# Optimization experiments

Measured on AMD Instinct MI355X. Metric: run time of the kernel, lower is better.

Reference implementation:

```python
import jax, jax.numpy as jnp
import numpy as np

RES = 320
B = 32

def make_trajectory():
    # Faithful to get_init_trajectory_full: grid points (i,j), zeroed inside the
    # skip bands (i in [140,170] OR j in [120,160]), then shifted by -res/2.
    I, J = np.meshgrid(np.arange(RES), np.arange(RES), indexing='ij')
    pts = np.stack([I, J], axis=-1).astype(np.float32)
    skip = ((I >= 140) & (I <= 170)) | ((J >= 120) & (J <= 160))
    pts[skip] = 0.0
    pts = pts.reshape(-1, 2) - 0.5 * RES
    return jnp.asarray(pts)

def setup_inputs():
    key = jax.random.key(0)
    k_space_input = jax.random.normal(key, (B, 1, RES, RES, 2), dtype=jnp.float32)
    trajectory = make_trajectory()
    return {"k_space_input": k_space_input, "trajectory": trajectory}

def _forward(k_space_input, trajectory):
    H = W = RES
    b = k_space_input.shape[0]
    # [B,1,H,W,2] -> permute(0,1,4,2,3).squeeze(1) -> [B,2,H,W]
    ksp = jnp.transpose(k_space_input[:, 0], (0, 3, 1, 2))
    c = ksp[:, 0] + 1j * ksp[:, 1]                       # [B,H,W] complex k-space

    # --- bilinear grid-sample at trajectory points (zero padding, align_corners=False) ---
    g = trajectory * (2.0 / W)                           # normalize [-res/2,res/2] -> [-1,1]
    x = ((g[:, 0] + 1.0) * W - 1.0) * 0.5                # pixel x (width)
    y = ((g[:, 1] + 1.0) * H - 1.0) * 0.5                # pixel y (height)
    x0f = jnp.floor(x); y0f = jnp.floor(y)
    fx = x - x0f; fy = y - y0f
    x0 = x0f.astype(jnp.int32); y0 = y0f.astype(jnp.int32)
    corners = ((x0,     y0,     (1 - fx) * (1 - fy)),
               (x0 + 1, y0,     fx       * (1 - fy)),
               (x0,     y0 + 1, (1 - fx) * fy),
               (x0 + 1, y0 + 1, fx       * fy))

    def gather(ix, iy):
        valid = (ix >= 0) & (ix < W) & (iy >= 0) & (iy < H)
        v = c[:, jnp.clip(iy, 0, H - 1), jnp.clip(ix, 0, W - 1)]   # [B,N]
        return jnp.where(valid[None, :], v, 0.0)

    sub = sum(gather(ix, iy) * w[None, :] for ix, iy, w in corners)  # [B,N] sampled k-space

    # --- NUFFT adjoint: bilinear gridding (adjoint scatter-add) + centered inverse FFT ---
    grid = jnp.zeros((b, H * W), dtype=sub.dtype)
    for ix, iy, w in corners:
        valid = (ix >= 0) & (ix < W) & (iy >= 0) & (iy < H)
        idx = jnp.clip(iy, 0, H - 1) * W + jnp.clip(ix, 0, W - 1)
        grid = grid.at[:, idx].add(sub * jnp.where(valid, w, 0.0)[None, :])
    kgrid = grid.reshape(b, H, W)
    img = jnp.fft.fftshift(
        jnp.fft.ifft2(jnp.fft.ifftshift(kgrid, axes=(-2, -1)), axes=(-2, -1)),
        axes=(-2, -1)) * (H * W)                          # adjoint DFT = N * centered ifft
    out = jnp.stack([img.real, img.imag], axis=1)         # [B,2,H,W]
    return out[:, None]                                   # unsqueeze(1) -> [B,1,2,H,W]

def reference(k_space_input, trajectory):
    return _forward(k_space_input, trajectory)
```

## Files before the change

### kernel.cpp

```cpp
#include <hip/hip_runtime.h>

#define RES 320
#define CELLS (RES * RES)
#define MDIM 640
#define NCOLS 10240
#define UF 192

#define DEGC 1360.625f

typedef __attribute__((ext_vector_type(8))) short short8;
typedef __attribute__((ext_vector_type(4))) float f32x4;

static __device__ __forceinline__ short f2bf(float f) {
    unsigned u = __builtin_bit_cast(unsigned, f);
    unsigned r = (u + 0x7fffu + ((u >> 16) & 1u)) >> 16;
    return (short)r;
}

#define GLD16(g, l) __builtin_amdgcn_global_load_lds(                        \
    (const __attribute__((address_space(1))) void*)(g),                      \
    (__attribute__((address_space(3))) void*)(l), 16, 0, 0)

__global__ __launch_bounds__(256) void gen_fafb(short* __restrict__ FBf,
                                                short* __restrict__ FAf) {
    int idx = blockIdx.x * 256 + threadIdx.x;
    int mat = idx / (2 * UF * RES);
    int r = idx - mat * (2 * UF * RES);
    int row = r / RES, c = r % RES;
    int plane = row >= UF;
    int n = row - UF * plane;
    float vr = 0.f;
    if (n <= 160) {
        int lo = mat ? 120 : 140, hi = mat ? 160 : 170;
#pragma unroll
        for (int dx = -1; dx <= 1; dx++) {
            int xx = c - dx;
            if (xx < 0 || xx > RES - 1) continue;
            int a0 = (xx < lo || xx > hi) ? 1 : 0;
            int a1 = (xx + 1 <= RES - 1 && (xx + 1 < lo || xx + 1 > hi)) ? 1 : 0;
            float w;
            if (dx == -1) w = (xx >= 1) ? (float)a0 : 0.f;
            else if (dx == 0) w = (float)(a0 + ((xx <= RES - 2) ? a1 : 0));
            else w = (xx <= RES - 2) ? (float)a1 : 0.f;
            if (w != 0.f) {
                int rr = (n * xx) % RES;
                float s, cc;
                sincospif((float)rr * (2.0f / RES), &s, &cc);
                float sign = ((n + xx) & 1) ? -1.0f : 1.0f;
                vr += w * sign * (plane ? s : cc);
            }
        }
        if (mat == 0) vr *= 0.0625f;
    }
    (mat ? FAf : FBf)[r] = f2bf(vr);
}

__global__ __launch_bounds__(256) void gemm1(const short* __restrict__ FBf,
                                             const float2* __restrict__ ksp,
                                             short* __restrict__ T) {
    __shared__ __align__(16) union {
        struct { short At[2][128 * 32]; short Bt[2][128 * 40]; } s;
        float Q[2][64 * 64];
    } sm;
    int tid = threadIdx.x;
    int lane = tid & 63, wave = tid >> 6;
    int wr = wave >> 1, wc = wave & 1;
    int d = blockIdx.x;
    int xcd = d & 7, rblk = d >> 3;
    int b = xcd * 4 + rblk / 15;
    int t5 = rblk % 15;
    int v0 = (t5 / 5) * 64;
    int y0b = (t5 % 5) * 64;
    const float2* kb = ksp + (size_t)b * CELLS;
    int q = lane >> 4, tl = lane & 15;
    int row4 = tid >> 2, ko = (tid & 3) * 8;
    int brow = tid >> 2, bxq = (tid & 3) * 8;
    f32x4 acc[4][4];
#pragma unroll
    for (int i = 0; i < 4; i++)
#pragma unroll
        for (int j = 0; j < 4; j++) acc[i][j] = {0.f, 0.f, 0.f, 0.f};

#define S1A(buf, k0)                                                         \
    {                                                                        \
        GLD16(FBf + (size_t)(v0 + row4) * RES + (k0) + ko,                   \
              sm.s.At[buf] + (size_t)(wave * 64) * 8);                       \
        GLD16(FBf + (size_t)(UF + v0 + row4) * RES + (k0) + ko,              \
              sm.s.At[buf] + (size_t)(256 + wave * 64) * 8);                 \
    }

    float2 bv[8];
#define S1BLOAD(k0)                                                          \
    {                                                                        \
        const float2* src = kb + (size_t)(y0b + brow) * RES + (k0) + bxq;    \
        _Pragma("unroll") for (int e = 0; e < 8; e++) bv[e] = src[e];        \
    }
#define S1BWRITE(buf)                                                        \
    {                                                                        \
        short8 r8, i8;                                                       \
        _Pragma("unroll") for (int e = 0; e < 8; e++) {                      \
            r8[e] = f2bf(bv[e].x);                                           \
            i8[e] = f2bf(bv[e].y);                                           \
        }                                                                    \
        *(short8*)&sm.s.Bt[buf][brow * 40 + bxq] = r8;                       \
        *(short8*)&sm.s.Bt[buf][(64 + brow) * 40 + bxq] = i8;                \
    }

    S1A(0, 0);
    S1BLOAD(0);
    S1BWRITE(0);
    __syncthreads();
    int cur = 0;
    for (int kt = 0; kt < 10; kt++) {
        if (kt < 9) {
            S1A(cur ^ 1, (kt + 1) * 32);
            S1BLOAD((kt + 1) * 32);
        }
        short8 a[4], bf[4];
#pragma unroll
        for (int i = 0; i < 4; i++)
            a[i] = *(const short8*)&sm.s.At[cur][(wr * 64 + i * 16 + tl) * 32 + q * 8];
#pragma unroll
        for (int j = 0; j < 4; j++)
            bf[j] = *(const short8*)&sm.s.Bt[cur][(wc * 64 + j * 16 + tl) * 40 + q * 8];
#pragma unroll
        for (int i = 0; i < 4; i++)
#pragma unroll
            for (int j = 0; j < 4; j++)
                acc[i][j] = __builtin_amdgcn_mfma_f32_16x16x32_bf16(a[i], bf[j], acc[i][j], 0, 0, 0);
        if (kt < 9) S1BWRITE(cur ^ 1);
        __syncthreads();
        cur ^= 1;
    }
    if (wave == 1 || wave == 3) {
        float* dst = sm.Q[wave >> 1];
#pragma unroll
        for (int i = 0; i < 4; i++)
#pragma unroll
            for (int j = 0; j < 4; j++)
#pragma unroll
                for (int t = 0; t < 4; t++)
                    dst[(i * 16 + q * 4 + t) * 64 + j * 16 + tl] = acc[i][j][t];
    }
    __syncthreads();
    if (wave == 0) {
#pragma unroll
        for (int i = 0; i < 4; i++)
#pragma unroll
            for (int j = 0; j < 4; j++)
#pragma unroll
                for (int t = 0; t < 4; t++) {
                    int r = i * 16 + q * 4 + t, cl = j * 16 + tl;
                    int n = v0 + r, y = y0b + cl;
                    float q11 = sm.Q[1][r * 64 + cl];
                    if (n <= 160)
                        T[(size_t)(b * RES + n) * MDIM + y] = f2bf(acc[i][j][t] - q11);
                    if (n >= 1 && n <= 159)
                        T[(size_t)(b * RES + RES - n) * MDIM + y] = f2bf(acc[i][j][t] + q11);
                }
    } else if (wave == 2) {
#pragma unroll
        for (int i = 0; i < 4; i++)
#pragma unroll
            for (int j = 0; j < 4; j++)
#pragma unroll
                for (int t = 0; t < 4; t++) {
                    int r = i * 16 + q * 4 + t, cl = j * 16 + tl;
                    int n = v0 + r, y = y0b + cl;
                    float q01 = sm.Q[0][r * 64 + cl];
                    if (n <= 160)
                        T[(size_t)(b * RES + n) * MDIM + RES + y] = f2bf(q01 + acc[i][j][t]);
                    if (n >= 1 && n <= 159)
                        T[(size_t)(b * RES + RES - n) * MDIM + RES + y] = f2bf(q01 - acc[i][j][t]);
                }
    }
}

__global__ __launch_bounds__(256) void gemm2(const short* __restrict__ T,
                                             const short* __restrict__ FAf,
                                             const float2* __restrict__ ksp,
                                             float* __restrict__ out) {
    __shared__ __align__(16) union {
        struct { short At[2][128 * 32]; short Bt[2][128 * 32]; } s;
        float Q[2][64 * 64];
    } sm;
    int tid = threadIdx.x;
    int lane = tid & 63, wave = tid >> 6;
    int wr = wave >> 1, wc = wave & 1;
    int d = blockIdx.x;
    int xcd = d & 7, rblk = d >> 3;
    int b = xcd * 4 + rblk / 15;
    int t5 = rblk % 15;
    int v0 = (t5 / 5) * 64;
    int n0b = (t5 % 5) * 64;
    int c0 = b * RES + n0b;
    int q = lane >> 4, tl = lane & 15;
    int row4 = tid >> 2, ko = (tid & 3) * 8;
    f32x4 acc[4][4];
#pragma unroll
    for (int i = 0; i < 4; i++)
#pragma unroll
        for (int j = 0; j < 4; j++) acc[i][j] = {0.f, 0.f, 0.f, 0.f};

#define S2(buf, k0)                                                          \
    {                                                                        \
        GLD16(FAf + (size_t)(v0 + row4) * RES + (k0) + ko,                   \
              sm.s.At[buf] + (size_t)(wave * 64) * 8);                       \
        GLD16(FAf + (size_t)(UF + v0 + row4) * RES + (k0) + ko,              \
              sm.s.At[buf] + (size_t)(256 + wave * 64) * 8);                 \
        GLD16(T + (size_t)(c0 + row4) * MDIM + (k0) + ko,                    \
              sm.s.Bt[buf] + (size_t)(wave * 64) * 8);                       \
        GLD16(T + (size_t)(c0 + row4) * MDIM + RES + (k0) + ko,              \
              sm.s.Bt[buf] + (size_t)(256 + wave * 64) * 8);                 \
    }

    S2(0, 0);
    __syncthreads();
    int cur = 0;
    for (int kt = 0; kt < 10; kt++) {
        if (kt < 9) S2(cur ^ 1, (kt + 1) * 32);
        short8 a[4], bf[4];
#pragma unroll
        for (int i = 0; i < 4; i++)
            a[i] = *(const short8*)&sm.s.At[cur][(wr * 64 + i * 16 + tl) * 32 + q * 8];
#pragma unroll
        for (int j = 0; j < 4; j++)
            bf[j] = *(const short8*)&sm.s.Bt[cur][(wc * 64 + j * 16 + tl) * 32 + q * 8];
#pragma unroll
        for (int i = 0; i < 4; i++)
#pragma unroll
            for (int j = 0; j < 4; j++)
                acc[i][j] = __builtin_amdgcn_mfma_f32_16x16x32_bf16(a[i], bf[j], acc[i][j], 0, 0, 0);
        __syncthreads();
        cur ^= 1;
    }
    if (wave == 1 || wave == 3) {
        float* dst = sm.Q[wave >> 1];
#pragma unroll
        for (int i = 0; i < 4; i++)
#pragma unroll
            for (int j = 0; j < 4; j++)
#pragma unroll
                for (int t = 0; t < 4; t++)
                    dst[(i * 16 + q * 4 + t) * 64 + j * 16 + tl] = acc[i][j][t];
    }
    __syncthreads();
    float2 g0 = ksp[(size_t)b * CELLS];
    if (wave == 0) {
        float g = DEGC * g0.x;
#pragma unroll
        for (int i = 0; i < 4; i++)
#pragma unroll
            for (int j = 0; j < 4; j++)
#pragma unroll
                for (int t = 0; t < 4; t++) {
                    int r = i * 16 + q * 4 + t, cl = j * 16 + tl;
                    int m = v0 + r, n = n0b + cl;
                    float q11 = sm.Q[1][r * 64 + cl];
                    float sgn = ((m + n) & 1) ? -1.0f : 1.0f;
                    size_t pb = (size_t)(b * 2) * RES;
                    if (m <= 160)
                        out[(pb + m) * RES + n] = (acc[i][j][t] - q11) + sgn * g;
                    if (m >= 1 && m <= 159)
                        out[(pb + RES - m) * RES + n] = (acc[i][j][t] + q11) + sgn * g;
                }
    } else if (wave == 2) {
        float g = DEGC * g0.y;
#pragma unroll
        for (int i = 0; i < 4; i++)
#pragma unroll
            for (int j = 0; j < 4; j++)
#pragma unroll
                for (int t = 0; t < 4; t++) {
                    int r = i * 16 + q * 4 + t, cl = j * 16 + tl;
                    int m = v0 + r, n = n0b + cl;
                    float q01 = sm.Q[0][r * 64 + cl];
                    float sgn = ((m + n) & 1) ? -1.0f : 1.0f;
                    size_t pb = (size_t)(b * 2 + 1) * RES;
                    if (m <= 160)
                        out[(pb + m) * RES + n] = (q01 + acc[i][j][t]) + sgn * g;
                    if (m >= 1 && m <= 159)
                        out[(pb + RES - m) * RES + n] = (q01 - acc[i][j][t]) + sgn * g;
                }
    }
}

extern "C" void kernel_launch(void* const* d_in, const int* in_sizes, int n_in,
                              void* d_out, int out_size, void* d_ws, size_t ws_size,
                              hipStream_t stream) {
    const float2* ksp = (const float2*)d_in[0];

    short* FBf = (short*)d_ws;
    short* FAf = FBf + (size_t)2 * UF * RES;
    short* T = FAf + (size_t)2 * UF * RES;

    gen_fafb<<<960, 256, 0, stream>>>(FBf, FAf);
    gemm1<<<480, 256, 0, stream>>>(FBf, ksp, T);
    gemm2<<<480, 256, 0, stream>>>(T, FAf, ksp, (float*)d_out);
}
```

Measured before the change: 108.2 us.

## Fuse both GEMM stages into one launch with per-batch atomic dependency counters

Merges the two GEMM kernels into one 960-block kernel. The first 480 blocks do stage one and increment a per-batch counter after writing T. The remaining blocks spin-wait until their batch's counter reaches 15, then run stage two. This is meant to remove the inter-kernel launch gap and the full-grid barrier, so stage two for early batches overlaps the stage-one tail. It adds a memset and spin-waits, and it relies on dispatch order for forward progress.

```diff
diff --git a/kernel.cpp b/kernel.cpp
--- a/kernel.cpp
+++ b/kernel.cpp
@@ -55,17 +55,14 @@
     (mat ? FAf : FBf)[r] = f2bf(vr);
 }
 
-__global__ __launch_bounds__(256) void gemm1(const short* __restrict__ FBf,
-                                             const float2* __restrict__ ksp,
-                                             short* __restrict__ T) {
-    __shared__ __align__(16) union {
-        struct { short At[2][128 * 32]; short Bt[2][128 * 40]; } s;
-        float Q[2][64 * 64];
-    } sm;
-    int tid = threadIdx.x;
+__device__ __forceinline__ void gemm1_body(const short* __restrict__ FBf,
+                                           const float2* __restrict__ ksp,
+                                           short* __restrict__ T,
+                                           unsigned* __restrict__ cnt,
+                                           int d, int tid,
+                                           short* At, short* Bt, float* Q) {
     int lane = tid & 63, wave = tid >> 6;
     int wr = wave >> 1, wc = wave & 1;
-    int d = blockIdx.x;
     int xcd = d & 7, rblk = d >> 3;
     int b = xcd * 4 + rblk / 15;
     int t5 = rblk % 15;
@@ -84,9 +81,9 @@
 #define S1A(buf, k0)                                                         \
     {                                                                        \
         GLD16(FBf + (size_t)(v0 + row4) * RES + (k0) + ko,                   \
-              sm.s.At[buf] + (size_t)(wave * 64) * 8);                       \
+              At + (size_t)(buf) * 4096 + (size_t)(wave * 64) * 8);          \
         GLD16(FBf + (size_t)(UF + v0 + row4) * RES + (k0) + ko,              \
-              sm.s.At[buf] + (size_t)(256 + wave * 64) * 8);                 \
+              At + (size_t)(buf) * 4096 + (size_t)(256 + wave * 64) * 8);    \
     }
 
     float2 bv[8];
@@ -102,8 +99,8 @@
             r8[e] = f2bf(bv[e].x);                                           \
             i8[e] = f2bf(bv[e].y);                                           \
         }                                                                    \
-        *(short8*)&sm.s.Bt[buf][brow * 40 + bxq] = r8;                       \
-        *(short8*)&sm.s.Bt[buf][(64 + brow) * 40 + bxq] = i8;                \
+        *(short8*)&Bt[(size_t)(buf) * 5120 + brow * 40 + bxq] = r8;          \
+        *(short8*)&Bt[(size_t)(buf) * 5120 + (64 + brow) * 40 + bxq] = i8;   \
     }
 
     S1A(0, 0);
@@ -119,10 +116,10 @@
         short8 a[4], bf[4];
 #pragma unroll
         for (int i = 0; i < 4; i++)
-            a[i] = *(const short8*)&sm.s.At[cur][(wr * 64 + i * 16 + tl) * 32 + q * 8];
+            a[i] = *(const short8*)&At[(size_t)cur * 4096 + (wr * 64 + i * 16 + tl) * 32 + q * 8];
 #pragma unroll
         for (int j = 0; j < 4; j++)
-            bf[j] = *(const short8*)&sm.s.Bt[cur][(wc * 64 + j * 16 + tl) * 40 + q * 8];
+            bf[j] = *(const short8*)&Bt[(size_t)cur * 5120 + (wc * 64 + j * 16 + tl) * 40 + q * 8];
 #pragma unroll
         for (int i = 0; i < 4; i++)
 #pragma unroll
@@ -132,8 +129,11 @@
         __syncthreads();
         cur ^= 1;
     }
+#undef S1A
+#undef S1BLOAD
+#undef S1BWRITE
     if (wave == 1 || wave == 3) {
-        float* dst = sm.Q[wave >> 1];
+        float* dst = Q + (size_t)(wave >> 1) * 4096;
 #pragma unroll
         for (int i = 0; i < 4; i++)
 #pragma unroll
@@ -152,7 +152,7 @@
                 for (int t = 0; t < 4; t++) {
                     int r = i * 16 + q * 4 + t, cl = j * 16 + tl;
                     int n = v0 + r, y = y0b + cl;
-                    float q11 = sm.Q[1][r * 64 + cl];
+                    float q11 = Q[4096 + r * 64 + cl];
                     if (n <= 160)
                         T[(size_t)(b * RES + n) * MDIM + y] = f2bf(acc[i][j][t] - q11);
                     if (n >= 1 && n <= 159)
@@ -167,27 +167,30 @@
                 for (int t = 0; t < 4; t++) {
                     int r = i * 16 + q * 4 + t, cl = j * 16 + tl;
                     int n = v0 + r, y = y0b + cl;
-                    float q01 = sm.Q[0][r * 64 + cl];
+                    float q01 = Q[r * 64 + cl];
                     if (n <= 160)
                         T[(size_t)(b * RES + n) * MDIM + RES + y] = f2bf(q01 + acc[i][j][t]);
                     if (n >= 1 && n <= 159)
                         T[(size_t)(b * RES + RES - n) * MDIM + RES + y] = f2bf(q01 - acc[i][j][t]);
                 }
     }
-}
-
-__global__ __launch_bounds__(256) void gemm2(const short* __restrict__ T,
-                                             const short* __restrict__ FAf,
-                                             const float2* __restrict__ ksp,
-                                             float* __restrict__ out) {
-    __shared__ __align__(16) union {
-        struct { short At[2][128 * 32]; short Bt[2][128 * 32]; } s;
-        float Q[2][64 * 64];
-    } sm;
-    int tid = threadIdx.x;
+    __syncthreads();
+    if (tid == 0) {
+        __threadfence();
+        __hip_atomic_fetch_add(&cnt[b], 1u, __ATOMIC_RELEASE,
+                               __HIP_MEMORY_SCOPE_AGENT);
+    }
+}
+
+__device__ __forceinline__ void gemm2_body(const short* __restrict__ T,
+                                           const short* __restrict__ FAf,
+                                           const float2* __restrict__ ksp,
+                                           float* __restrict__ out,
+                                           unsigned* __restrict__ cnt,
+                                           int d, int tid,
+                                           short* At, short* Bt, float* Q) {
     int lane = tid & 63, wave = tid >> 6;
     int wr = wave >> 1, wc = wave & 1;
-    int d = blockIdx.x;
     int xcd = d & 7, rblk = d >> 3;
     int b = xcd * 4 + rblk / 15;
     int t5 = rblk % 15;
@@ -196,6 +199,15 @@
     int c0 = b * RES + n0b;
     int q = lane >> 4, tl = lane & 15;
     int row4 = tid >> 2, ko = (tid & 3) * 8;
+
+    if (tid == 0) {
+        while (__hip_atomic_load(&cnt[b], __ATOMIC_ACQUIRE,
+                                 __HIP_MEMORY_SCOPE_AGENT) < 15u)
+            __builtin_amdgcn_s_sleep(8);
+        __threadfence();
+    }
+    __syncthreads();
+
     f32x4 acc[4][4];
 #pragma unroll
     for (int i = 0; i < 4; i++)
@@ -205,13 +217,13 @@
 #define S2(buf, k0)                                                          \
     {                                                                        \
         GLD16(FAf + (size_t)(v0 + row4) * RES + (k0) + ko,                   \
-              sm.s.At[buf] + (size_t)(wave * 64) * 8);                       \
+              At + (size_t)(buf) * 4096 + (size_t)(wave * 64) * 8);          \
         GLD16(FAf + (size_t)(UF + v0 + row4) * RES + (k0) + ko,              \
-              sm.s.At[buf] + (size_t)(256 + wave * 64) * 8);                 \
+              At + (size_t)(buf) * 4096 + (size_t)(256 + wave * 64) * 8);    \
         GLD16(T + (size_t)(c0 + row4) * MDIM + (k0) + ko,                    \
-              sm.s.Bt[buf] + (size_t)(wave * 64) * 8);                       \
+              Bt + (size_t)(buf) * 4096 + (size_t)(wave * 64) * 8);          \
         GLD16(T + (size_t)(c0 + row4) * MDIM + RES + (k0) + ko,              \
-              sm.s.Bt[buf] + (size_t)(256 + wave * 64) * 8);                 \
+              Bt + (size_t)(buf) * 4096 + (size_t)(256 + wave * 64) * 8);    \
     }
 
     S2(0, 0);
@@ -222,10 +234,10 @@
         short8 a[4], bf[4];
 #pragma unroll
         for (int i = 0; i < 4; i++)
-            a[i] = *(const short8*)&sm.s.At[cur][(wr * 64 + i * 16 + tl) * 32 + q * 8];
+            a[i] = *(const short8*)&At[(size_t)cur * 4096 + (wr * 64 + i * 16 + tl) * 32 + q * 8];
 #pragma unroll
         for (int j = 0; j < 4; j++)
-            bf[j] = *(const short8*)&sm.s.Bt[cur][(wc * 64 + j * 16 + tl) * 32 + q * 8];
+            bf[j] = *(const short8*)&Bt[(size_t)cur * 4096 + (wc * 64 + j * 16 + tl) * 32 + q * 8];
 #pragma unroll
         for (int i = 0; i < 4; i++)
 #pragma unroll
@@ -234,8 +246,9 @@
         __syncthreads();
         cur ^= 1;
     }
+#undef S2
     if (wave == 1 || wave == 3) {
-        float* dst = sm.Q[wave >> 1];
+        float* dst = Q + (size_t)(wave >> 1) * 4096;
 #pragma unroll
         for (int i = 0; i < 4; i++)
 #pragma unroll
@@ -256,7 +269,7 @@
                 for (int t = 0; t < 4; t++) {
                     int r = i * 16 + q * 4 + t, cl = j * 16 + tl;
                     int m = v0 + r, n = n0b + cl;
-                    float q11 = sm.Q[1][r * 64 + cl];
+                    float q11 = Q[4096 + r * 64 + cl];
                     float sgn = ((m + n) & 1) ? -1.0f : 1.0f;
                     size_t pb = (size_t)(b * 2) * RES;
                     if (m <= 160)
@@ -274,7 +287,7 @@
                 for (int t = 0; t < 4; t++) {
                     int r = i * 16 + q * 4 + t, cl = j * 16 + tl;
                     int m = v0 + r, n = n0b + cl;
-                    float q01 = sm.Q[0][r * 64 + cl];
+                    float q01 = Q[r * 64 + cl];
                     float sgn = ((m + n) & 1) ? -1.0f : 1.0f;
                     size_t pb = (size_t)(b * 2 + 1) * RES;
                     if (m <= 160)
@@ -285,6 +298,23 @@
     }
 }
 
+__global__ __launch_bounds__(256) void gemm_fused(
+    const short* __restrict__ FBf, const short* __restrict__ FAf,
+    const float2* __restrict__ ksp, short* __restrict__ T,
+    float* __restrict__ out, unsigned* __restrict__ cnt) {
+    __shared__ __align__(16) union {
+        struct { short At[2 * 128 * 32]; short Bt[2 * 128 * 40]; } g1;
+        struct { short At[2 * 128 * 32]; short Bt[2 * 128 * 32]; } g2;
+        float Q[2 * 64 * 64];
+    } sm;
+    int tid = threadIdx.x;
+    if (blockIdx.x < 480)
+        gemm1_body(FBf, ksp, T, cnt, blockIdx.x, tid, sm.g1.At, sm.g1.Bt, sm.Q);
+    else
+        gemm2_body(T, FAf, ksp, out, cnt, blockIdx.x - 480, tid,
+                   sm.g2.At, sm.g2.Bt, sm.Q);
+}
+
 extern "C" void kernel_launch(void* const* d_in, const int* in_sizes, int n_in,
                               void* d_out, int out_size, void* d_ws, size_t ws_size,
                               hipStream_t stream) {
@@ -293,8 +323,9 @@
     short* FBf = (short*)d_ws;
     short* FAf = FBf + (size_t)2 * UF * RES;
     short* T = FAf + (size_t)2 * UF * RES;
-
+    unsigned* cnt = (unsigned*)(T + (size_t)NCOLS * MDIM);
+
+    hipMemsetAsync(cnt, 0, 32 * sizeof(unsigned), stream);
     gen_fafb<<<960, 256, 0, stream>>>(FBf, FAf);
-    gemm1<<<480, 256, 0, stream>>>(FBf, ksp, T);
-    gemm2<<<480, 256, 0, stream>>>(T, FAf, ksp, (float*)d_out);
-}
+    gemm_fused<<<960, 256, 0, stream>>>(FBf, FAf, ksp, T, (float*)d_out, cnt);
+}
```

New measurement: 252.2 us. 2.33x slower.
